# Kernel optimization log

Hardware: AMD Instinct MI355X
Metric: run time of the kernel (lower is better)

Reference implementation:

```python
import jax, jax.numpy as jnp
import numpy as np

B, H, SQ, SK, D, DV = 2, 16, 2048, 2048, 64, 64
SCALE_FACTOR = 2.0   # non-standard: applied AFTER softmax as 1/scale_factor
DROPOUT_P = 0.1
DROPOUT_KEY = 42     # fixed key -> deterministic dropout mask


def setup_inputs() -> dict:
    key = jax.random.key(0)
    kq, kk, kv = jax.random.split(key, 3)
    return {
        "query": jax.random.normal(kq, (B, H, SQ, D), dtype=jnp.float32),
        "k": jax.random.normal(kk, (H, SK, D), dtype=jnp.float32),
        "v": jax.random.normal(kv, (H, SK, DV), dtype=jnp.float32),
    }


def reference(query, k, v):
    # qk = query @ k^T : [B,H,Sq,Sk]
    qk = jnp.einsum("bhqd,hkd->bhqk", query, k)
    inv_scale = 1.0 / SCALE_FACTOR
    probs = jax.nn.softmax(qk, axis=-1) * inv_scale
    # dropout (train mode, inverted-dropout scaling), deterministic mask
    keep = jax.random.bernoulli(jax.random.key(DROPOUT_KEY), 1.0 - DROPOUT_P, probs.shape)
    probs = jnp.where(keep, probs / (1.0 - DROPOUT_P), 0.0)
    # output = probs @ v : [B,H,Sq,Dv]
    return jnp.einsum("bhqk,hkv->bhqv", probs, v)
```

## Files before the change

### kernel.cpp

```cpp
#include <hip/hip_runtime.h>
#include <stdint.h>
#include <math.h>

namespace {
constexpr int Bb = 2, Hh = 16, SQc = 2048, SKc = 2048, Dc = 64, DVc = 64;
constexpr int TK = 64;
constexpr float LOG2E = 1.4426950408889634f;
constexpr uint64_t KEEP_T = 0xE666666666667000ull;

typedef __attribute__((ext_vector_type(8))) short short8;
typedef __attribute__((ext_vector_type(4))) float f32x4;

__device__ __forceinline__ uint32_t rotl_(uint32_t x, int r) {
  return __builtin_amdgcn_alignbit(x, x, 32 - r);
}

__device__ __forceinline__ uint64_t tf_bits64(uint32_t ctr) {
  const uint32_t KS1 = 42u, KS2 = 0x1BD11BF0u;
  uint32_t x0, x1;
  x1 = ctr + KS1;
  x0 = x1;        x1 = rotl_(x1, 13); x1 ^= x0;
  x0 += x1;       x1 = rotl_(x1, 15); x1 ^= x0;
  x0 += x1;       x1 = rotl_(x1, 26); x1 ^= x0;
  x0 += x1;       x1 = rotl_(x1,  6); x1 ^= x0;
  x1 += KS2 + 1u;
  x0 += KS1 + x1; x1 = rotl_(x1, 17); x1 ^= x0;
  x0 += x1;       x1 = rotl_(x1, 29); x1 ^= x0;
  x0 += x1;       x1 = rotl_(x1, 16); x1 ^= x0;
  x0 += x1;       x1 = rotl_(x1, 24); x1 ^= x0;
  x1 += 2u;
  x0 += KS2 + x1; x1 = rotl_(x1, 13); x1 ^= x0;
  x0 += x1;       x1 = rotl_(x1, 15); x1 ^= x0;
  x0 += x1;       x1 = rotl_(x1, 26); x1 ^= x0;
  x0 += x1;       x1 = rotl_(x1,  6); x1 ^= x0;
  x1 += KS1 + 3u;
  x0 += x1;       x1 = rotl_(x1, 17); x1 ^= x0;
  x0 += x1;       x1 = rotl_(x1, 29); x1 ^= x0;
  x0 += x1;       x1 = rotl_(x1, 16); x1 ^= x0;
  x0 += x1;       x1 = rotl_(x1, 24); x1 ^= x0;
  x1 += KS2 + 4u;
  x0 += KS1 + x1; x1 = rotl_(x1, 13); x1 ^= x0;
  x0 += x1;       x1 = rotl_(x1, 15); x1 ^= x0;
  x0 += x1;       x1 = rotl_(x1, 26); x1 ^= x0;
  x0 += x1;       x1 = rotl_(x1,  6); x1 ^= x0;
  return ((uint64_t)(x0 + KS2) << 32) | (uint64_t)(x1 + 5u);
}

__device__ __forceinline__ uint32_t f2bf_u(float x) {
  uint32_t u = __float_as_uint(x);
  u += 0x7FFFu + ((u >> 16) & 1u);
  return u >> 16;
}

__device__ __forceinline__ void gl_lds16(const void* g, void* l) {
  __builtin_amdgcn_global_load_lds(
      (const __attribute__((address_space(1))) unsigned int*)g,
      (__attribute__((address_space(3))) unsigned int*)l, 16, 0, 0);
}
}

__global__ __launch_bounds__(256) void prep_kernel(
    const float* __restrict__ k, const float* __restrict__ v,
    unsigned short* __restrict__ Khg, unsigned short* __restrict__ Klg,
    unsigned short* __restrict__ Vtg) {
  __shared__ float Vs[64 * 65];
  const int t = threadIdx.x;
  const int h = blockIdx.x >> 5;
  const int kt = blockIdx.x & 31;
  const size_t src = ((size_t)h * SKc + kt * 64) * Dc;
  const size_t tb = (size_t)(h * 32 + kt) * 4096;
#pragma unroll
  for (int i = 0; i < 4; ++i) {
    int idx = t + 256 * i;
    int row = idx >> 4, d0 = (idx & 15) << 2;
    float4 kv = *(const float4*)(k + src + row * Dc + d0);
    uint32_t hx = f2bf_u(kv.x), hy = f2bf_u(kv.y), hz = f2bf_u(kv.z), hw = f2bf_u(kv.w);
    uint32_t lx = f2bf_u(kv.x - __uint_as_float(hx << 16));
    uint32_t ly = f2bf_u(kv.y - __uint_as_float(hy << 16));
    uint32_t lz = f2bf_u(kv.z - __uint_as_float(hz << 16));
    uint32_t lw = f2bf_u(kv.w - __uint_as_float(hw << 16));
    int phys = row * 64 + (((d0 >> 3) ^ (row & 7)) << 3) + (d0 & 7);
    *(ushort4*)(Khg + tb + phys) =
        make_ushort4((unsigned short)hx, (unsigned short)hy, (unsigned short)hz, (unsigned short)hw);
    *(ushort4*)(Klg + tb + phys) =
        make_ushort4((unsigned short)lx, (unsigned short)ly, (unsigned short)lz, (unsigned short)lw);
    float4 vv = *(const float4*)(v + src + row * Dc + d0);
    *(float4*)(&Vs[row * 65 + d0]) = vv;
  }
  __syncthreads();
  const int dv = t >> 2;
  const int j0 = (t & 3) << 1;
#pragma unroll
  for (int g = 0; g < 2; ++g) {
    int chunk = j0 + g;
    unsigned short tmp[8];
#pragma unroll
    for (int s = 0; s < 8; ++s)
      tmp[s] = (unsigned short)f2bf_u(Vs[(chunk * 8 + s) * 65 + dv]);
    *(short8*)(Vtg + tb + dv * 64 + ((chunk ^ (dv & 7)) << 3)) = *(const short8*)tmp;
  }
}

__global__ __launch_bounds__(512, 6) void attn_main(
    const float* __restrict__ q, const unsigned short* __restrict__ Khg,
    const unsigned short* __restrict__ Klg, const unsigned short* __restrict__ Vtg,
    float* __restrict__ out) {
  __shared__ __align__(16) unsigned short stag[2][12288];

  const int t = threadIdx.x;
  const int lane = t & 63;
  const int w = t >> 6;
  const int lm = lane & 15;
  const int quad = lane >> 4;
  const int khalf = w & 1;
  const int qsub = w >> 1;

  const int vid = (blockIdx.x & 7) * 128 + (blockIdx.x >> 3);
  const int qt = vid & 31;
  const int h = (vid >> 5) & 15;
  const int b = vid >> 9;
  const int qrow = qt * 64 + qsub * 16 + lm;

  short8 qh[2], ql[2];
  {
    const float* qp = q + (((size_t)(b * Hh + h)) * SQc + qrow) * Dc;
#pragma unroll
    for (int c = 0; c < 2; ++c) {
#pragma unroll
      for (int j2 = 0; j2 < 2; ++j2) {
        float4 x = *(const float4*)(qp + c * 32 + quad * 8 + j2 * 4);
        float xs[4] = {x.x * LOG2E, x.y * LOG2E, x.z * LOG2E, x.w * LOG2E};
#pragma unroll
        for (int j = 0; j < 4; ++j) {
          uint32_t hb = f2bf_u(xs[j]);
          float lo = xs[j] - __uint_as_float(hb << 16);
          qh[c][j2 * 4 + j] = (short)hb;
          ql[c][j2 * 4 + j] = (short)f2bf_u(lo);
        }
      }
    }
  }

  const char* kh_t = (const char*)Khg + (size_t)(h * 32) * 8192;
  const char* kl_t = (const char*)Klg + (size_t)(h * 32) * 8192;
  const char* vt_t = (const char*)Vtg + (size_t)(h * 32) * 8192;
  unsigned short* sb = &stag[khalf][0];

  f32x4 acc[4] = {{0.f, 0.f, 0.f, 0.f}, {0.f, 0.f, 0.f, 0.f},
                  {0.f, 0.f, 0.f, 0.f}, {0.f, 0.f, 0.f, 0.f}};
  float l_i = 0.f;

  const int e = lm & 7;
  const int a0s = lm * 64 + ((quad ^ e) << 3);
  const int a1s = lm * 64 + (((quad + 4) ^ e) << 3);

  const int pa0 = ((quad & 1) * 32 + lm) << 2;
  const int pa1 = pa0 + 64;
  const uint32_t sel = (quad >= 2) ? 0x07060302u : 0x05040100u;

  uint32_t ctile = ((uint32_t)((b * Hh + h) * SQc + qrow)) * (uint32_t)SKc +
                   (uint32_t)(khalf * 16 * TK + quad * 4);

#pragma unroll 1
  for (int i = 0; i < 16; ++i, ctile += TK) {
    const int kt = khalf * 16 + i;
    __syncthreads();
    {
      const size_t tile = (size_t)kt * 8192;
#pragma unroll
      for (int r = 0; r < 2; ++r) {
        int off = r * 4096 + qsub * 1024 + lane * 16;
        gl_lds16(kh_t + tile + off, (char*)sb + off);
        gl_lds16(kl_t + tile + off, (char*)sb + 8192 + off);
        gl_lds16(vt_t + tile + off, (char*)sb + 16384 + off);
      }
    }
    __syncthreads();

#pragma unroll
    for (int c = 0; c < 2; ++c) {
      f32x4 s0 = {0.f, 0.f, 0.f, 0.f}, s1 = {0.f, 0.f, 0.f, 0.f};
#pragma unroll
      for (int d = 0; d < 2; ++d) {
        const int ad = (d == 0) ? a0s : a1s;
        short8 kh0 = *(const short8*)&sb[ad + (2 * c) * 1024];
        short8 kl0 = *(const short8*)&sb[ad + (2 * c) * 1024 + 4096];
        s0 = __builtin_amdgcn_mfma_f32_16x16x32_bf16(kh0, qh[d], s0, 0, 0, 0);
        s0 = __builtin_amdgcn_mfma_f32_16x16x32_bf16(kl0, qh[d], s0, 0, 0, 0);
        s0 = __builtin_amdgcn_mfma_f32_16x16x32_bf16(kh0, ql[d], s0, 0, 0, 0);
        short8 kh1 = *(const short8*)&sb[ad + (2 * c + 1) * 1024];
        short8 kl1 = *(const short8*)&sb[ad + (2 * c + 1) * 1024 + 4096];
        s1 = __builtin_amdgcn_mfma_f32_16x16x32_bf16(kh1, qh[d], s1, 0, 0, 0);
        s1 = __builtin_amdgcn_mfma_f32_16x16x32_bf16(kl1, qh[d], s1, 0, 0, 0);
        s1 = __builtin_amdgcn_mfma_f32_16x16x32_bf16(kh1, ql[d], s1, 0, 0, 0);
      }

      uint32_t pkc[4];
#pragma unroll
      for (int r = 0; r < 4; ++r) {
        float p0 = __builtin_amdgcn_exp2f(s0[r]);
        float p1 = __builtin_amdgcn_exp2f(s1[r]);
        l_i += p0 + p1;
        uint64_t b0 = tf_bits64(ctile + (uint32_t)(c * 32 + r));
        uint64_t b1 = tf_bits64(ctile + (uint32_t)(c * 32 + 16 + r));
        float k0 = (b0 < KEEP_T) ? p0 : 0.0f;
        float k1 = (b1 < KEEP_T) ? p1 : 0.0f;
        uint32_t pk;
        asm("v_cvt_pk_bf16_f32 %0, %1, %2" : "=v"(pk) : "v"(k0), "v"(k1));
        pkc[r] = pk;
      }

      short8 pb;
      {
        uint32_t e0 = (uint32_t)__builtin_amdgcn_ds_bpermute(pa0, (int)pkc[0]);
        uint32_t e1 = (uint32_t)__builtin_amdgcn_ds_bpermute(pa0, (int)pkc[1]);
        uint32_t e2 = (uint32_t)__builtin_amdgcn_ds_bpermute(pa0, (int)pkc[2]);
        uint32_t e3 = (uint32_t)__builtin_amdgcn_ds_bpermute(pa0, (int)pkc[3]);
        uint32_t f0 = (uint32_t)__builtin_amdgcn_ds_bpermute(pa1, (int)pkc[0]);
        uint32_t f1 = (uint32_t)__builtin_amdgcn_ds_bpermute(pa1, (int)pkc[1]);
        uint32_t f2 = (uint32_t)__builtin_amdgcn_ds_bpermute(pa1, (int)pkc[2]);
        uint32_t f3 = (uint32_t)__builtin_amdgcn_ds_bpermute(pa1, (int)pkc[3]);
        uint32_t w0 = __builtin_amdgcn_perm(e1, e0, sel);
        uint32_t w1 = __builtin_amdgcn_perm(e3, e2, sel);
        uint32_t w2 = __builtin_amdgcn_perm(f1, f0, sel);
        uint32_t w3 = __builtin_amdgcn_perm(f3, f2, sel);
        uint32_t tmp[4] = {w0, w1, w2, w3};
        pb = *(const short8*)tmp;
      }

      {
        const int ac = (c == 0) ? a0s : a1s;
#pragma unroll
        for (int nb = 0; nb < 4; ++nb) {
          short8 vb = *(const short8*)&sb[ac + nb * 1024 + 8192];
          acc[nb] = __builtin_amdgcn_mfma_f32_16x16x32_bf16(vb, pb, acc[nb], 0, 0, 0);
        }
      }
    }
  }

  l_i += __shfl_xor(l_i, 16);
  l_i += __shfl_xor(l_i, 32);

  float (*Lacc)[16][72] = (float(*)[16][72])&stag[0][0];
  float* Ll = (float*)((char*)&stag[0][0] + 18432);
  __syncthreads();
  if (khalf == 1) {
#pragma unroll
    for (int nb = 0; nb < 4; ++nb)
      *(f32x4*)&Lacc[qsub][lm][nb * 16 + quad * 4] = acc[nb];
    if (quad == 0) Ll[qsub * 16 + lm] = l_i;
  }
  __syncthreads();
  if (khalf == 0) {
    float lt = l_i + Ll[qsub * 16 + lm];
    float sc = (0.5f / 0.9f) / lt;
    float* op = out + (((size_t)(b * Hh + h)) * SQc + qrow) * DVc;
#pragma unroll
    for (int nb = 0; nb < 4; ++nb) {
      f32x4 other = *(const f32x4*)&Lacc[qsub][lm][nb * 16 + quad * 4];
      float4 o = make_float4((acc[nb][0] + other[0]) * sc, (acc[nb][1] + other[1]) * sc,
                             (acc[nb][2] + other[2]) * sc, (acc[nb][3] + other[3]) * sc);
      *(float4*)(op + nb * 16 + quad * 4) = o;
    }
  }
}

extern "C" void kernel_launch(void* const* d_in, const int* in_sizes, int n_in,
                              void* d_out, int out_size, void* d_ws, size_t ws_size,
                              hipStream_t stream) {
  const float* q = (const float*)d_in[0];
  const float* k = (const float*)d_in[1];
  const float* v = (const float*)d_in[2];
  float* out = (float*)d_out;
  unsigned short* Khg = (unsigned short*)d_ws;
  unsigned short* Klg = Khg + (size_t)Hh * SKc * Dc;
  unsigned short* Vtg = Klg + (size_t)Hh * SKc * Dc;
  prep_kernel<<<dim3(Hh * 32), 256, 0, stream>>>(k, v, Khg, Klg, Vtg);
  attn_main<<<dim3(Bb * Hh * (SQc / 64)), 512, 0, stream>>>(q, Khg, Klg, Vtg, out);
}
```

Before: 360.8 us.

## Read K/V tiles directly from global memory instead of LDS staging

Removes the global-to-LDS staging of the bf16 K-high, K-low and transposed V tiles, along with the two block barriers per iteration. Each wave now loads its MFMA operands straight from global memory, relying on L1/L2 caches for reuse across the four q-subtile waves that share a tile. LDS shrinks to the final reduction buffers and the launch-bounds occupancy hint rises from 6 to 8. The trade-off is more global and cache traffic plus exposed load latency with no explicit prefetch, against fewer barriers and higher occupancy.

```diff
diff --git a/kernel.cpp b/kernel.cpp
--- a/kernel.cpp
+++ b/kernel.cpp
@@ -51,12 +51,6 @@
   u += 0x7FFFu + ((u >> 16) & 1u);
   return u >> 16;
 }
-
-__device__ __forceinline__ void gl_lds16(const void* g, void* l) {
-  __builtin_amdgcn_global_load_lds(
-      (const __attribute__((address_space(1))) unsigned int*)g,
-      (__attribute__((address_space(3))) unsigned int*)l, 16, 0, 0);
-}
 }
 
 __global__ __launch_bounds__(256) void prep_kernel(
@@ -101,11 +95,12 @@
   }
 }
 
-__global__ __launch_bounds__(512, 6) void attn_main(
+__global__ __launch_bounds__(512, 8) void attn_main(
     const float* __restrict__ q, const unsigned short* __restrict__ Khg,
     const unsigned short* __restrict__ Klg, const unsigned short* __restrict__ Vtg,
     float* __restrict__ out) {
-  __shared__ __align__(16) unsigned short stag[2][12288];
+  __shared__ __align__(16) float Lacc[4][16][72];
+  __shared__ float Ll[64];
 
   const int t = threadIdx.x;
   const int lane = t & 63;
@@ -141,10 +136,10 @@
     }
   }
 
-  const char* kh_t = (const char*)Khg + (size_t)(h * 32) * 8192;
-  const char* kl_t = (const char*)Klg + (size_t)(h * 32) * 8192;
-  const char* vt_t = (const char*)Vtg + (size_t)(h * 32) * 8192;
-  unsigned short* sb = &stag[khalf][0];
+  const size_t tsh = (size_t)(h * 32 + khalf * 16) * 4096;
+  const unsigned short* pKh = Khg + tsh;
+  const unsigned short* pKl = Klg + tsh;
+  const unsigned short* pVt = Vtg + tsh;
 
   f32x4 acc[4] = {{0.f, 0.f, 0.f, 0.f}, {0.f, 0.f, 0.f, 0.f},
                   {0.f, 0.f, 0.f, 0.f}, {0.f, 0.f, 0.f, 0.f}};
@@ -162,34 +157,20 @@
                    (uint32_t)(khalf * 16 * TK + quad * 4);
 
 #pragma unroll 1
-  for (int i = 0; i < 16; ++i, ctile += TK) {
-    const int kt = khalf * 16 + i;
-    __syncthreads();
-    {
-      const size_t tile = (size_t)kt * 8192;
-#pragma unroll
-      for (int r = 0; r < 2; ++r) {
-        int off = r * 4096 + qsub * 1024 + lane * 16;
-        gl_lds16(kh_t + tile + off, (char*)sb + off);
-        gl_lds16(kl_t + tile + off, (char*)sb + 8192 + off);
-        gl_lds16(vt_t + tile + off, (char*)sb + 16384 + off);
-      }
-    }
-    __syncthreads();
-
+  for (int i = 0; i < 16; ++i, ctile += TK, pKh += 4096, pKl += 4096, pVt += 4096) {
 #pragma unroll
     for (int c = 0; c < 2; ++c) {
       f32x4 s0 = {0.f, 0.f, 0.f, 0.f}, s1 = {0.f, 0.f, 0.f, 0.f};
 #pragma unroll
       for (int d = 0; d < 2; ++d) {
         const int ad = (d == 0) ? a0s : a1s;
-        short8 kh0 = *(const short8*)&sb[ad + (2 * c) * 1024];
-        short8 kl0 = *(const short8*)&sb[ad + (2 * c) * 1024 + 4096];
+        short8 kh0 = *(const short8*)&pKh[ad + (2 * c) * 1024];
+        short8 kl0 = *(const short8*)&pKl[ad + (2 * c) * 1024];
         s0 = __builtin_amdgcn_mfma_f32_16x16x32_bf16(kh0, qh[d], s0, 0, 0, 0);
         s0 = __builtin_amdgcn_mfma_f32_16x16x32_bf16(kl0, qh[d], s0, 0, 0, 0);
         s0 = __builtin_amdgcn_mfma_f32_16x16x32_bf16(kh0, ql[d], s0, 0, 0, 0);
-        short8 kh1 = *(const short8*)&sb[ad + (2 * c + 1) * 1024];
-        short8 kl1 = *(const short8*)&sb[ad + (2 * c + 1) * 1024 + 4096];
+        short8 kh1 = *(const short8*)&pKh[ad + (2 * c + 1) * 1024];
+        short8 kl1 = *(const short8*)&pKl[ad + (2 * c + 1) * 1024];
         s1 = __builtin_amdgcn_mfma_f32_16x16x32_bf16(kh1, qh[d], s1, 0, 0, 0);
         s1 = __builtin_amdgcn_mfma_f32_16x16x32_bf16(kl1, qh[d], s1, 0, 0, 0);
         s1 = __builtin_amdgcn_mfma_f32_16x16x32_bf16(kh1, ql[d], s1, 0, 0, 0);
@@ -232,7 +213,7 @@
         const int ac = (c == 0) ? a0s : a1s;
 #pragma unroll
         for (int nb = 0; nb < 4; ++nb) {
-          short8 vb = *(const short8*)&sb[ac + nb * 1024 + 8192];
+          short8 vb = *(const short8*)&pVt[ac + nb * 1024];
           acc[nb] = __builtin_amdgcn_mfma_f32_16x16x32_bf16(vb, pb, acc[nb], 0, 0, 0);
         }
       }
@@ -242,9 +223,6 @@
   l_i += __shfl_xor(l_i, 16);
   l_i += __shfl_xor(l_i, 32);
 
-  float (*Lacc)[16][72] = (float(*)[16][72])&stag[0][0];
-  float* Ll = (float*)((char*)&stag[0][0] + 18432);
-  __syncthreads();
   if (khalf == 1) {
 #pragma unroll
     for (int nb = 0; nb < 4; ++nb)
```

Result: slower. 625.7 us (+73.5%).

## Double-buffer K/V tiles and give each wave its own query rows

Applied to the files above, without the earlier changes.

The key-split across two wave halves is dropped. Each of the 8 waves now owns 16 query rows and walks all 32 key tiles, so each block covers 128 query rows and the grid halves. The two LDS buffers become a double buffer: the next tile's async global-to-LDS load is issued before computing the current one, which removes one barrier per iteration along with the cross-half reduction epilogue. The cost is twice as many serial iterations per wave, fewer blocks, and a lower occupancy hint in launch bounds.

```diff
diff --git a/kernel.cpp b/kernel.cpp
--- a/kernel.cpp
+++ b/kernel.cpp
@@ -101,7 +101,7 @@
   }
 }
 
-__global__ __launch_bounds__(512, 6) void attn_main(
+__global__ __launch_bounds__(512, 4) void attn_main(
     const float* __restrict__ q, const unsigned short* __restrict__ Khg,
     const unsigned short* __restrict__ Klg, const unsigned short* __restrict__ Vtg,
     float* __restrict__ out) {
@@ -112,14 +112,12 @@
   const int w = t >> 6;
   const int lm = lane & 15;
   const int quad = lane >> 4;
-  const int khalf = w & 1;
-  const int qsub = w >> 1;
-
-  const int vid = (blockIdx.x & 7) * 128 + (blockIdx.x >> 3);
-  const int qt = vid & 31;
-  const int h = (vid >> 5) & 15;
-  const int b = vid >> 9;
-  const int qrow = qt * 64 + qsub * 16 + lm;
+
+  const int vid = (blockIdx.x & 7) * 64 + (blockIdx.x >> 3);
+  const int qt = vid & 15;
+  const int h = (vid >> 4) & 15;
+  const int b = vid >> 8;
+  const int qrow = qt * 128 + w * 16 + lm;
 
   short8 qh[2], ql[2];
   {
@@ -144,7 +142,6 @@
   const char* kh_t = (const char*)Khg + (size_t)(h * 32) * 8192;
   const char* kl_t = (const char*)Klg + (size_t)(h * 32) * 8192;
   const char* vt_t = (const char*)Vtg + (size_t)(h * 32) * 8192;
-  unsigned short* sb = &stag[khalf][0];
 
   f32x4 acc[4] = {{0.f, 0.f, 0.f, 0.f}, {0.f, 0.f, 0.f, 0.f},
                   {0.f, 0.f, 0.f, 0.f}, {0.f, 0.f, 0.f, 0.f}};
@@ -159,23 +156,28 @@
   const uint32_t sel = (quad >= 2) ? 0x07060302u : 0x05040100u;
 
   uint32_t ctile = ((uint32_t)((b * Hh + h) * SQc + qrow)) * (uint32_t)SKc +
-                   (uint32_t)(khalf * 16 * TK + quad * 4);
+                   (uint32_t)(quad * 4);
+
+  const int soff = w * 1024 + lane * 16;
+
+  {
+    char* db = (char*)&stag[0][0];
+    gl_lds16(kh_t + soff, db + soff);
+    gl_lds16(kl_t + soff, db + 8192 + soff);
+    gl_lds16(vt_t + soff, db + 16384 + soff);
+  }
 
 #pragma unroll 1
-  for (int i = 0; i < 16; ++i, ctile += TK) {
-    const int kt = khalf * 16 + i;
+  for (int i = 0; i < 32; ++i, ctile += TK) {
     __syncthreads();
-    {
-      const size_t tile = (size_t)kt * 8192;
-#pragma unroll
-      for (int r = 0; r < 2; ++r) {
-        int off = r * 4096 + qsub * 1024 + lane * 16;
-        gl_lds16(kh_t + tile + off, (char*)sb + off);
-        gl_lds16(kl_t + tile + off, (char*)sb + 8192 + off);
-        gl_lds16(vt_t + tile + off, (char*)sb + 16384 + off);
-      }
+    if (i < 31) {
+      const size_t tile = (size_t)(i + 1) * 8192;
+      char* db = (char*)&stag[(i & 1) ^ 1][0];
+      gl_lds16(kh_t + tile + soff, db + soff);
+      gl_lds16(kl_t + tile + soff, db + 8192 + soff);
+      gl_lds16(vt_t + tile + soff, db + 16384 + soff);
     }
-    __syncthreads();
+    const unsigned short* sb = &stag[i & 1][0];
 
 #pragma unroll
     for (int c = 0; c < 2; ++c) {
@@ -241,28 +243,13 @@
 
   l_i += __shfl_xor(l_i, 16);
   l_i += __shfl_xor(l_i, 32);
-
-  float (*Lacc)[16][72] = (float(*)[16][72])&stag[0][0];
-  float* Ll = (float*)((char*)&stag[0][0] + 18432);
-  __syncthreads();
-  if (khalf == 1) {
-#pragma unroll
-    for (int nb = 0; nb < 4; ++nb)
-      *(f32x4*)&Lacc[qsub][lm][nb * 16 + quad * 4] = acc[nb];
-    if (quad == 0) Ll[qsub * 16 + lm] = l_i;
-  }
-  __syncthreads();
-  if (khalf == 0) {
-    float lt = l_i + Ll[qsub * 16 + lm];
-    float sc = (0.5f / 0.9f) / lt;
-    float* op = out + (((size_t)(b * Hh + h)) * SQc + qrow) * DVc;
-#pragma unroll
-    for (int nb = 0; nb < 4; ++nb) {
-      f32x4 other = *(const f32x4*)&Lacc[qsub][lm][nb * 16 + quad * 4];
-      float4 o = make_float4((acc[nb][0] + other[0]) * sc, (acc[nb][1] + other[1]) * sc,
-                             (acc[nb][2] + other[2]) * sc, (acc[nb][3] + other[3]) * sc);
-      *(float4*)(op + nb * 16 + quad * 4) = o;
-    }
+  const float sc = (0.5f / 0.9f) / l_i;
+  float* op = out + (((size_t)(b * Hh + h)) * SQc + qrow) * DVc;
+#pragma unroll
+  for (int nb = 0; nb < 4; ++nb) {
+    float4 o = make_float4(acc[nb][0] * sc, acc[nb][1] * sc,
+                           acc[nb][2] * sc, acc[nb][3] * sc);
+    *(float4*)(op + nb * 16 + quad * 4) = o;
   }
 }
 
@@ -277,5 +264,5 @@
   unsigned short* Klg = Khg + (size_t)Hh * SKc * Dc;
   unsigned short* Vtg = Klg + (size_t)Hh * SKc * Dc;
   prep_kernel<<<dim3(Hh * 32), 256, 0, stream>>>(k, v, Khg, Klg, Vtg);
-  attn_main<<<dim3(Bb * Hh * (SQc / 64)), 512, 0, stream>>>(q, Khg, Klg, Vtg, out);
-}
+  attn_main<<<dim3(Bb * Hh * (SQc / 128)), 512, 0, stream>>>(q, Khg, Klg, Vtg, out);
+}
```

Result: no change. 358.4 us (-0.7%).
